# Kernel tuning notes

Hardware: AMD Instinct MI355X
Metric: run time of the kernel (lower is better)

Reference implementation:

```python
import jax, jax.numpy as jnp
import numpy as np

DIM = 768
NUM_HEADS = 12
HEAD_DIM = DIM // NUM_HEADS
SCALE = HEAD_DIM ** -0.5
NEG = -9e15


def setup_inputs() -> dict:
    key = jax.random.key(0)
    ks = jax.random.split(key, 8)
    B, N, M, C = 4, 1024, 2048, DIM
    q = jax.random.normal(ks[0], (B, N, C), dtype=jnp.float32)
    kv = jax.random.normal(ks[1], (B, M, C), dtype=jnp.float32)
    mask = jax.random.randint(ks[2], (B, 1, N, M), 0, 2, dtype=jnp.int32)
    s = 1.0 / np.sqrt(C)
    Wq = jax.random.normal(ks[3], (C, C), dtype=jnp.float32) * s      # nn.Linear(dim, dim), no bias
    Wkv = jax.random.normal(ks[4], (2 * C, C), dtype=jnp.float32) * s  # nn.Linear(dim, 2*dim), no bias
    Wproj = jax.random.normal(ks[5], (C, C), dtype=jnp.float32) * s
    bproj = jax.random.normal(ks[6], (C,), dtype=jnp.float32) * s
    return {"q": q, "kv": kv, "Wq": Wq, "Wkv": Wkv, "Wproj": Wproj, "bproj": bproj, "mask": mask}


def reference(q, kv, Wq, Wkv, Wproj, bproj, mask):
    B, M, C = kv.shape
    _, N, _ = q.shape
    H, d = NUM_HEADS, HEAD_DIM
    # kv projection -> [B, M, 2, H, d] -> k, v: [B, H, M, d]
    kvp = (kv @ Wkv.T).reshape(B, M, 2, H, d)
    k = kvp[:, :, 0].transpose(0, 2, 1, 3)
    v = kvp[:, :, 1].transpose(0, 2, 1, 3)
    # q projection -> [B, H, N, d], pre-scaled
    qp = (q @ Wq.T).reshape(B, N, H, d).transpose(0, 2, 1, 3) * SCALE
    attn = jnp.einsum('bhnd,bhmd->bhnm', qp, k)  # [B, H, N, M]
    attn = jnp.where(mask == 0, NEG, attn)
    attn = jax.nn.softmax(attn, axis=-1)
    # attn_drop / proj_drop have rate 0.0 (eval): identity
    x = jnp.einsum('bhnm,bhmd->bhnd', attn, v)
    x = x.transpose(0, 2, 1, 3).reshape(B, N, C)
    x = x @ Wproj.T + bproj
    return x
```

## Files before the change

kernel.cpp:

```cpp
#include <hip/hip_runtime.h>
#include <hip/hip_bf16.h>


typedef short    s16x8  __attribute__((ext_vector_type(8)));
typedef short    s16x4  __attribute__((ext_vector_type(4)));
typedef float    f32x4  __attribute__((ext_vector_type(4)));
typedef _Float16 f16x8  __attribute__((ext_vector_type(8)));
typedef _Float16 f16x4  __attribute__((ext_vector_type(4)));
typedef _Float16 f16x2  __attribute__((ext_vector_type(2)));

#define NUM_H 12
#define DIM   768
#define NQ    1024
#define MK    2048
#define QK_SCALE_LOG2E 0.18033688f

__device__ __forceinline__ short f2h(float v) {
    _Float16 h = (_Float16)v;
    return __builtin_bit_cast(short, h);
}
__device__ __forceinline__ f32x4 mfma16x32(f16x8 a, f16x8 b, f32x4 c) {
    return __builtin_amdgcn_mfma_f32_16x16x32_f16(a, b, c, 0, 0, 0);
}
__device__ __forceinline__ f32x4 mfma16x16(f16x4 a, f16x4 b, f32x4 c) {
    return __builtin_amdgcn_mfma_f32_16x16x16f16(a, b, c, 0, 0, 0);
}
__device__ __forceinline__ f16x2 pk2h(float a, float b) {
    return __builtin_bit_cast(f16x2, __builtin_amdgcn_cvt_pkrtz(a, b));
}

__global__ __launch_bounds__(256) void prep_kernel(
    const float* __restrict__ q, const float* __restrict__ kv,
    const float* __restrict__ Wq, const float* __restrict__ Wkv,
    const float* __restrict__ Wp, const int* __restrict__ mask,
    short* __restrict__ q_h, short* __restrict__ kv_h,
    short* __restrict__ Wq_h, short* __restrict__ Wkv_h,
    short* __restrict__ Wp_h, unsigned char* __restrict__ mbytes)
{
    int bid = blockIdx.x;
    if (bid < 5760) {
        const float* s; short* d; long base;
        if (bid < 1536)      { s = q;   d = q_h;   base = (long)bid * 2048; }
        else if (bid < 4608) { s = kv;  d = kv_h;  base = (long)(bid - 1536) * 2048; }
        else if (bid < 4896) { s = Wq;  d = Wq_h;  base = (long)(bid - 4608) * 2048; }
        else if (bid < 5472) { s = Wkv; d = Wkv_h; base = (long)(bid - 4896) * 2048; }
        else                 { s = Wp;  d = Wp_h;  base = (long)(bid - 5472) * 2048; }
        long i = base + threadIdx.x * 8;
        float4 a = *(const float4*)(s + i);
        float4 b = *(const float4*)(s + i + 4);
        s16x8 r;
        r[0] = f2h(a.x); r[1] = f2h(a.y); r[2] = f2h(a.z); r[3] = f2h(a.w);
        r[4] = f2h(b.x); r[5] = f2h(b.y); r[6] = f2h(b.z); r[7] = f2h(b.w);
        *(s16x8*)(d + i) = r;
    } else {
        long base = (long)(bid - 5760) * 2048 + threadIdx.x * 8;
        int4 m0 = *(const int4*)(mask + base);
        int4 m1 = *(const int4*)(mask + base + 4);
        unsigned v = (unsigned)(m0.x != 0)        | ((unsigned)(m0.y != 0) << 1)
                   | ((unsigned)(m0.z != 0) << 2) | ((unsigned)(m0.w != 0) << 3)
                   | ((unsigned)(m1.x != 0) << 4) | ((unsigned)(m1.y != 0) << 5)
                   | ((unsigned)(m1.z != 0) << 6) | ((unsigned)(m1.w != 0) << 7);
        mbytes[base >> 3] = (unsigned char)v;
    }
}

__device__ __forceinline__ void gemm_core(
    short* smem,
    const short* __restrict__ A, const short* __restrict__ Bt,
    int Ncols, int mode, const float* __restrict__ bias,
    short* __restrict__ outb, short* __restrict__ outb2,
    float* __restrict__ outf, int bid)
{
    short (*As)[72] = (short(*)[72])smem;
    short (*Bs)[72] = (short(*)[72])(smem + 9216);

    int ntiles = Ncols >> 7;
    int m0 = (bid / ntiles) << 7;
    int n0 = (bid % ntiles) << 7;
    int t = threadIdx.x;
    int w = t >> 6, lane = t & 63, quad = lane >> 4, l16 = lane & 15;
    int wm = (w & 1) << 6, wn = (w >> 1) << 6;

    f32x4 zero4 = {0.f, 0.f, 0.f, 0.f};
    f32x4 acc[4][4];
    for (int i = 0; i < 4; i++)
        for (int j = 0; j < 4; j++) acc[i][j] = zero4;

    int lr = t >> 1;
    int lc = (t & 1) << 5;
    const short* Ap = A + (long)(m0 + lr) * DIM + lc;
    const short* Bp = Bt + (long)(n0 + lr) * DIM + lc;

    s16x8 a8[4], b8[4];
    #pragma unroll
    for (int c = 0; c < 4; c++) {
        a8[c] = *(const s16x8*)(Ap + c * 8);
        b8[c] = *(const s16x8*)(Bp + c * 8);
    }

    for (int kt = 0; kt < DIM; kt += 64) {
        __syncthreads();
        #pragma unroll
        for (int c = 0; c < 4; c++) {
            *(s16x8*)&As[lr][lc + c * 8] = a8[c];
            *(s16x8*)&Bs[lr][lc + c * 8] = b8[c];
        }
        __syncthreads();
        if (kt + 64 < DIM) {
            #pragma unroll
            for (int c = 0; c < 4; c++) {
                a8[c] = *(const s16x8*)(Ap + kt + 64 + c * 8);
                b8[c] = *(const s16x8*)(Bp + kt + 64 + c * 8);
            }
        }
        #pragma unroll
        for (int kh = 0; kh < 2; kh++) {
            f16x8 af[4], bfr[4];
            #pragma unroll
            for (int i = 0; i < 4; i++) {
                s16x8 tmp = *(const s16x8*)&As[wm + i * 16 + l16][kh * 32 + quad * 8];
                af[i] = __builtin_bit_cast(f16x8, tmp);
            }
            #pragma unroll
            for (int j = 0; j < 4; j++) {
                s16x8 tmp = *(const s16x8*)&Bs[wn + j * 16 + l16][kh * 32 + quad * 8];
                bfr[j] = __builtin_bit_cast(f16x8, tmp);
            }
            #pragma unroll
            for (int i = 0; i < 4; i++)
                #pragma unroll
                for (int j = 0; j < 4; j++)
                    acc[i][j] = mfma16x32(af[i], bfr[j], acc[i][j]);
        }
    }

    __syncthreads();

    if (mode == 2) {
        #pragma unroll
        for (int i = 0; i < 4; i++)
            #pragma unroll
            for (int j = 0; j < 4; j++)
                #pragma unroll
                for (int r = 0; r < 4; r++) {
                    int row = m0 + wm + i * 16 + quad * 4 + r;
                    int col = n0 + wn + j * 16 + l16;
                    outf[(long)row * DIM + col] = acc[i][j][r] + bias[col];
                }
        return;
    }

    short (*Cs)[136] = (short(*)[136])smem;
    bool vreg = (mode == 1) && (n0 >= DIM);

    if (!vreg) {
        float sc = (mode == 0) ? QK_SCALE_LOG2E : 1.0f;
        #pragma unroll
        for (int i = 0; i < 4; i++)
            #pragma unroll
            for (int j = 0; j < 4; j++)
                #pragma unroll
                for (int r = 0; r < 4; r++)
                    Cs[wm + i * 16 + quad * 4 + r][wn + j * 16 + l16] =
                        f2h(acc[i][j][r] * sc);
    } else {
        #pragma unroll
        for (int i = 0; i < 4; i++)
            #pragma unroll
            for (int j = 0; j < 4; j++) {
                int c = wn + j * 16 + l16;
                int r0 = wm + i * 16 + quad * 4;
                s16x4 pk;
                pk[0] = f2h(acc[i][j][0]); pk[1] = f2h(acc[i][j][1]);
                pk[2] = f2h(acc[i][j][2]); pk[3] = f2h(acc[i][j][3]);
                *(s16x4*)&Cs[c][r0] = pk;
            }
    }
    __syncthreads();

    if (!vreg) {
        int hb2 = n0 >> 6;
        long rowsN = (mode == 0) ? NQ : MK;
        int b = (int)(m0 / rowsN);
        int rb = (int)(m0 % rowsN);
        short* ob0 = outb + ((long)(b * NUM_H + hb2) * rowsN + rb) * 64;
        short* ob1 = outb + ((long)(b * NUM_H + hb2 + 1) * rowsN + rb) * 64;
        #pragma unroll
        for (int k2 = 0; k2 < 8; k2++) {
            int ch = k2 * 256 + t;
            int half = ch >> 10, off = ch & 1023;
            s16x8 vd = *(const s16x8*)&Cs[off >> 3][(half << 6) + ((off & 7) << 3)];
            *(s16x8*)((half ? ob1 : ob0) + off * 8) = vd;
        }
    } else {
        int hb2 = (n0 - DIM) >> 6;
        int b = m0 >> 11, rb = m0 & 2047;
        #pragma unroll
        for (int k2 = 0; k2 < 8; k2++) {
            int ch = k2 * 256 + t;
            int c = ch >> 4, woff = (ch & 15) << 3;
            s16x8 vd = *(const s16x8*)&Cs[c][woff];
            int half = c >> 6, dd = c & 63;
            *(s16x8*)(outb2 + (((long)(b * NUM_H + hb2 + half) * 64 + dd) * MK + rb) + woff) = vd;
        }
    }
}

__global__ __launch_bounds__(256) void gemm12_kernel(
    const short* __restrict__ qh, const short* __restrict__ Wqh,
    const short* __restrict__ kvh, const short* __restrict__ Wkvh,
    short* __restrict__ qp, short* __restrict__ kk, short* __restrict__ vt)
{
    __shared__ short smem[18432];
    if (blockIdx.x < 192)
        gemm_core(smem, qh, Wqh, 768, 0, nullptr, qp, nullptr, nullptr, blockIdx.x);
    else
        gemm_core(smem, kvh, Wkvh, 1536, 1, nullptr, kk, vt, nullptr, blockIdx.x - 192);
}

__global__ __launch_bounds__(256) void gemm3_kernel(
    const short* __restrict__ xb, const short* __restrict__ Wph,
    const float* __restrict__ bias, float* __restrict__ out)
{
    __shared__ short smem[18432];
    gemm_core(smem, xb, Wph, 768, 2, bias, nullptr, nullptr, out, blockIdx.x);
}

__global__ __launch_bounds__(128) void attn_kernel(
    const short* __restrict__ qp, const short* __restrict__ kk,
    const short* __restrict__ vt, const unsigned* __restrict__ mb,
    short* __restrict__ xb)
{
    __shared__ short qs[64][72];
    __shared__ short ks[64][72];
    __shared__ short vs[64][72];

    int bid = blockIdx.x;
    int bh = bid % 48;
    int nt = bid / 48;
    int h = bh % NUM_H, b = bh / NUM_H;
    int n0 = nt << 6;
    int t = threadIdx.x, w = t >> 6, lane = t & 63, quad = lane >> 4, l16 = lane & 15;

    const short* qbase = qp + ((long)bh * NQ + n0) * 64;
    const short* kbase = kk + (long)bh * MK * 64;
    const short* vbase = vt + (long)bh * 64 * MK;
    const unsigned* mrow0 = mb + ((long)b * NQ + n0 + (w << 5) + l16) * 64;
    const unsigned* mrow1 = mrow0 + 16 * 64;

    int gr = t >> 3, gc = (t & 7) << 3;
    #pragma unroll
    for (int i = 0; i < 4; i++)
        *(s16x8*)&qs[gr + i * 16][gc] = *(const s16x8*)(qbase + (gr + i * 16) * 64 + gc);
    __syncthreads();

    f16x8 bq[2][2];
    #pragma unroll
    for (int s2 = 0; s2 < 2; s2++)
        #pragma unroll
        for (int kh = 0; kh < 2; kh++)
            bq[s2][kh] = __builtin_bit_cast(f16x8,
                *(const s16x8*)&qs[(w << 5) + (s2 << 4) + l16][kh * 32 + quad * 8]);

    s16x8 k8[4], v8[4];
    #pragma unroll
    for (int i = 0; i < 4; i++) {
        k8[i] = *(const s16x8*)(kbase + (long)(gr + i * 16) * 64 + gc);
        v8[i] = *(const s16x8*)(vbase + (long)(gr + i * 16) * MK + gc);
    }
    uint2 mw0 = *(const uint2*)(mrow0);
    uint2 mw1 = *(const uint2*)(mrow1);

    f32x4 zero4 = {0.f, 0.f, 0.f, 0.f};
    f32x4 o[2][4], ol[2];
    #pragma unroll
    for (int s2 = 0; s2 < 2; s2++) {
        ol[s2] = zero4;
        for (int j = 0; j < 4; j++) o[s2][j] = zero4;
    }
    const f16x4 ones = {(_Float16)1.f, (_Float16)1.f, (_Float16)1.f, (_Float16)1.f};

    for (int mt = 0; mt < MK; mt += 64) {
        __syncthreads();
        #pragma unroll
        for (int i = 0; i < 4; i++) {
            *(s16x8*)&ks[gr + i * 16][gc] = k8[i];
            *(s16x8*)&vs[gr + i * 16][gc] = v8[i];
        }
        unsigned cm[2][2] = {{mw0.x, mw0.y}, {mw1.x, mw1.y}};
        __syncthreads();
        if (mt + 64 < MK) {
            #pragma unroll
            for (int i = 0; i < 4; i++) {
                k8[i] = *(const s16x8*)(kbase + (long)(mt + 64 + gr + i * 16) * 64 + gc);
                v8[i] = *(const s16x8*)(vbase + (long)(gr + i * 16) * MK + mt + 64 + gc);
            }
            mw0 = *(const uint2*)(mrow0 + ((mt + 64) >> 5));
            mw1 = *(const uint2*)(mrow1 + ((mt + 64) >> 5));
        }

        f32x4 s[2][4];
        #pragma unroll
        for (int j = 0; j < 4; j++) { s[0][j] = zero4; s[1][j] = zero4; }
        #pragma unroll
        for (int kh = 0; kh < 2; kh++)
            #pragma unroll
            for (int j = 0; j < 4; j++) {
                f16x8 ak = __builtin_bit_cast(f16x8,
                    *(const s16x8*)&ks[j * 16 + l16][kh * 32 + quad * 8]);
                s[0][j] = mfma16x32(ak, bq[0][kh], s[0][j]);
                s[1][j] = mfma16x32(ak, bq[1][kh], s[1][j]);
            }

        f16x4 pa[2][4];
        #pragma unroll
        for (int s2 = 0; s2 < 2; s2++)
            #pragma unroll
            for (int j = 0; j < 4; j++) {
                unsigned wsel = (j < 2) ? cm[s2][0] : cm[s2][1];
                unsigned bits = wsel >> (((j & 1) << 4) + (quad << 2));
                float p0 = (bits & 1u)        ? __builtin_amdgcn_exp2f(s[s2][j][0]) : 0.f;
                float p1 = ((bits >> 1) & 1u) ? __builtin_amdgcn_exp2f(s[s2][j][1]) : 0.f;
                float p2 = ((bits >> 2) & 1u) ? __builtin_amdgcn_exp2f(s[s2][j][2]) : 0.f;
                float p3 = ((bits >> 3) & 1u) ? __builtin_amdgcn_exp2f(s[s2][j][3]) : 0.f;
                f16x2 lo = pk2h(p0, p1);
                f16x2 hi = pk2h(p2, p3);
                pa[s2][j] = __builtin_shufflevector(lo, hi, 0, 1, 2, 3);
            }

        #pragma unroll
        for (int j = 0; j < 4; j++) {
            ol[0] = mfma16x16(pa[0][j], ones, ol[0]);
            ol[1] = mfma16x16(pa[1][j], ones, ol[1]);
            #pragma unroll
            for (int jd = 0; jd < 4; jd++) {
                f16x4 bv = *(const f16x4*)&vs[jd * 16 + l16][j * 16 + quad * 4];
                o[0][jd] = mfma16x16(pa[0][j], bv, o[0][jd]);
                o[1][jd] = mfma16x16(pa[1][j], bv, o[1][jd]);
            }
        }
    }

    #pragma unroll
    for (int s2 = 0; s2 < 2; s2++) {
        float linv[4];
        #pragma unroll
        for (int rr = 0; rr < 4; rr++) linv[rr] = 1.0f / ol[s2][rr];
        #pragma unroll
        for (int jd = 0; jd < 4; jd++)
            #pragma unroll
            for (int rr = 0; rr < 4; rr++)
                qs[(w << 5) + (s2 << 4) + quad * 4 + rr][jd * 16 + l16] =
                    f2h(o[s2][jd][rr] * linv[rr]);
    }
    __syncthreads();
    #pragma unroll
    for (int k2 = 0; k2 < 4; k2++) {
        int row = (w << 5) + (lane >> 3) + k2 * 8;
        int cc = (lane & 7) << 3;
        s16x8 vd = *(const s16x8*)&qs[row][cc];
        *(s16x8*)(xb + ((long)b * NQ + n0 + row) * DIM + h * 64 + cc) = vd;
    }
}

extern "C" void kernel_launch(void* const* d_in, const int* in_sizes, int n_in,
                              void* d_out, int out_size, void* d_ws, size_t ws_size,
                              hipStream_t stream)
{
    const float* q     = (const float*)d_in[0];
    const float* kv    = (const float*)d_in[1];
    const float* Wq    = (const float*)d_in[2];
    const float* Wkv   = (const float*)d_in[3];
    const float* Wproj = (const float*)d_in[4];
    const float* bproj = (const float*)d_in[5];
    const int*   mask  = (const int*)d_in[6];
    float* out = (float*)d_out;

    char* ws = (char*)d_ws;
    short* q_h   = (short*)ws; ws += (size_t)4096 * 768 * 2;
    short* kv_h  = (short*)ws; ws += (size_t)8192 * 768 * 2;
    short* Wq_h  = (short*)ws; ws += (size_t)768 * 768 * 2;
    short* Wkv_h = (short*)ws; ws += (size_t)1536 * 768 * 2;
    short* Wp_h  = (short*)ws; ws += (size_t)768 * 768 * 2;
    short* qp    = (short*)ws; ws += (size_t)4096 * 768 * 2;
    short* kk    = (short*)ws; ws += (size_t)8192 * 768 * 2;
    short* vt    = (short*)ws; ws += (size_t)8192 * 768 * 2;
    short* xb    = (short*)ws; ws += (size_t)4096 * 768 * 2;
    unsigned char* mbytes = (unsigned char*)ws;

    prep_kernel<<<9856, 256, 0, stream>>>(q, kv, Wq, Wkv, Wproj, mask,
                                          q_h, kv_h, Wq_h, Wkv_h, Wp_h, mbytes);
    gemm12_kernel<<<960, 256, 0, stream>>>(q_h, Wq_h, kv_h, Wkv_h, qp, kk, vt);
    attn_kernel<<<768, 128, 0, stream>>>(qp, kk, vt, (const unsigned*)mbytes, xb);
    gemm3_kernel<<<192, 256, 0, stream>>>(xb, Wp_h, bproj, out);
}
```

Measured before the change: 226.5 us.

## Use 4 waves per attention block and 16x16x32 MFMA for PV

The attention kernel goes from 2 waves with 32 query rows each to 4 waves with 16 query rows each, doubling threads per block for the same 64-row tile. K rows are stored into shared memory with a permuted row order, so the score MFMA output lanes line up with the A-operand layout of a 16x16x32 MFMA. That lets the PV and row-sum products use the wider K=32 instruction instead of 16x16x16. The intent is more latency hiding and fewer MFMA issues. In exchange each wave reuses less of K/V from shared memory, and correctness depends on the permutation matching the mask bit layout.

New measurement: 216.4 us. 1.05x faster.

```diff
diff --git a/kernel.cpp b/kernel.cpp
--- a/kernel.cpp
+++ b/kernel.cpp
@@ -21,9 +21,6 @@
 }
 __device__ __forceinline__ f32x4 mfma16x32(f16x8 a, f16x8 b, f32x4 c) {
     return __builtin_amdgcn_mfma_f32_16x16x32_f16(a, b, c, 0, 0, 0);
-}
-__device__ __forceinline__ f32x4 mfma16x16(f16x4 a, f16x4 b, f32x4 c) {
-    return __builtin_amdgcn_mfma_f32_16x16x16f16(a, b, c, 0, 0, 0);
 }
 __device__ __forceinline__ f16x2 pk2h(float a, float b) {
     return __builtin_bit_cast(f16x2, __builtin_amdgcn_cvt_pkrtz(a, b));
@@ -226,7 +223,7 @@
     gemm_core(smem, xb, Wph, 768, 2, bias, nullptr, nullptr, out, blockIdx.x);
 }
 
-__global__ __launch_bounds__(128) void attn_kernel(
+__global__ __launch_bounds__(256) void attn_kernel(
     const short* __restrict__ qp, const short* __restrict__ kk,
     const short* __restrict__ vt, const unsigned* __restrict__ mb,
     short* __restrict__ xb)
@@ -245,121 +242,114 @@
     const short* qbase = qp + ((long)bh * NQ + n0) * 64;
     const short* kbase = kk + (long)bh * MK * 64;
     const short* vbase = vt + (long)bh * 64 * MK;
-    const unsigned* mrow0 = mb + ((long)b * NQ + n0 + (w << 5) + l16) * 64;
-    const unsigned* mrow1 = mrow0 + 16 * 64;
-
-    int gr = t >> 3, gc = (t & 7) << 3;
-    #pragma unroll
-    for (int i = 0; i < 4; i++)
-        *(s16x8*)&qs[gr + i * 16][gc] = *(const s16x8*)(qbase + (gr + i * 16) * 64 + gc);
+    const unsigned* mrow = mb + ((long)b * NQ + n0 + (w << 4) + l16) * 64;
+
+    {
+        int qr = t >> 2, c0 = (t & 3) << 4;
+        *(s16x8*)&qs[qr][c0]     = *(const s16x8*)(qbase + qr * 64 + c0);
+        *(s16x8*)&qs[qr][c0 + 8] = *(const s16x8*)(qbase + qr * 64 + c0 + 8);
+    }
     __syncthreads();
-
-    f16x8 bq[2][2];
-    #pragma unroll
-    for (int s2 = 0; s2 < 2; s2++)
-        #pragma unroll
-        for (int kh = 0; kh < 2; kh++)
-            bq[s2][kh] = __builtin_bit_cast(f16x8,
-                *(const s16x8*)&qs[(w << 5) + (s2 << 4) + l16][kh * 32 + quad * 8]);
-
-    s16x8 k8[4], v8[4];
-    #pragma unroll
-    for (int i = 0; i < 4; i++) {
-        k8[i] = *(const s16x8*)(kbase + (long)(gr + i * 16) * 64 + gc);
-        v8[i] = *(const s16x8*)(vbase + (long)(gr + i * 16) * MK + gc);
-    }
-    uint2 mw0 = *(const uint2*)(mrow0);
-    uint2 mw1 = *(const uint2*)(mrow1);
+    f16x8 bq[2];
+    #pragma unroll
+    for (int kh = 0; kh < 2; kh++)
+        bq[kh] = __builtin_bit_cast(f16x8,
+            *(const s16x8*)&qs[(w << 4) + l16][kh * 32 + quad * 8]);
+
+    int sr = t >> 2, c0 = (t & 3) << 4;
+    int pr = (sr & 32) + ((sr & 4) << 2) + ((sr & 24) >> 1) + (sr & 3);
+    const short* kp = kbase + (long)sr * 64 + c0;
+    const short* vp = vbase + (long)sr * MK + c0;
+
+    s16x8 k0 = *(const s16x8*)(kp);
+    s16x8 k1 = *(const s16x8*)(kp + 8);
+    s16x8 v0 = *(const s16x8*)(vp);
+    s16x8 v1 = *(const s16x8*)(vp + 8);
+    uint2 mwv = *(const uint2*)(mrow);
 
     f32x4 zero4 = {0.f, 0.f, 0.f, 0.f};
-    f32x4 o[2][4], ol[2];
-    #pragma unroll
-    for (int s2 = 0; s2 < 2; s2++) {
-        ol[s2] = zero4;
-        for (int j = 0; j < 4; j++) o[s2][j] = zero4;
-    }
-    const f16x4 ones = {(_Float16)1.f, (_Float16)1.f, (_Float16)1.f, (_Float16)1.f};
+    f32x4 o[4], ol = zero4;
+    for (int j = 0; j < 4; j++) o[j] = zero4;
+    const f16x8 ones = {(_Float16)1.f, (_Float16)1.f, (_Float16)1.f, (_Float16)1.f,
+                        (_Float16)1.f, (_Float16)1.f, (_Float16)1.f, (_Float16)1.f};
 
     for (int mt = 0; mt < MK; mt += 64) {
         __syncthreads();
-        #pragma unroll
-        for (int i = 0; i < 4; i++) {
-            *(s16x8*)&ks[gr + i * 16][gc] = k8[i];
-            *(s16x8*)&vs[gr + i * 16][gc] = v8[i];
-        }
-        unsigned cm[2][2] = {{mw0.x, mw0.y}, {mw1.x, mw1.y}};
+        *(s16x8*)&ks[pr][c0]     = k0;
+        *(s16x8*)&ks[pr][c0 + 8] = k1;
+        *(s16x8*)&vs[sr][c0]     = v0;
+        *(s16x8*)&vs[sr][c0 + 8] = v1;
+        unsigned cm0 = mwv.x, cm1 = mwv.y;
         __syncthreads();
         if (mt + 64 < MK) {
-            #pragma unroll
-            for (int i = 0; i < 4; i++) {
-                k8[i] = *(const s16x8*)(kbase + (long)(mt + 64 + gr + i * 16) * 64 + gc);
-                v8[i] = *(const s16x8*)(vbase + (long)(gr + i * 16) * MK + mt + 64 + gc);
-            }
-            mw0 = *(const uint2*)(mrow0 + ((mt + 64) >> 5));
-            mw1 = *(const uint2*)(mrow1 + ((mt + 64) >> 5));
-        }
-
-        f32x4 s[2][4];
-        #pragma unroll
-        for (int j = 0; j < 4; j++) { s[0][j] = zero4; s[1][j] = zero4; }
+            k0 = *(const s16x8*)(kp + (long)(mt + 64) * 64);
+            k1 = *(const s16x8*)(kp + (long)(mt + 64) * 64 + 8);
+            v0 = *(const s16x8*)(vp + mt + 64);
+            v1 = *(const s16x8*)(vp + mt + 64 + 8);
+            mwv = *(const uint2*)(mrow + ((mt + 64) >> 5));
+        }
+
+        f32x4 s[4];
+        #pragma unroll
+        for (int jj = 0; jj < 4; jj++) s[jj] = zero4;
         #pragma unroll
         for (int kh = 0; kh < 2; kh++)
             #pragma unroll
-            for (int j = 0; j < 4; j++) {
+            for (int jj = 0; jj < 4; jj++) {
                 f16x8 ak = __builtin_bit_cast(f16x8,
-                    *(const s16x8*)&ks[j * 16 + l16][kh * 32 + quad * 8]);
-                s[0][j] = mfma16x32(ak, bq[0][kh], s[0][j]);
-                s[1][j] = mfma16x32(ak, bq[1][kh], s[1][j]);
-            }
-
-        f16x4 pa[2][4];
-        #pragma unroll
-        for (int s2 = 0; s2 < 2; s2++)
-            #pragma unroll
-            for (int j = 0; j < 4; j++) {
-                unsigned wsel = (j < 2) ? cm[s2][0] : cm[s2][1];
-                unsigned bits = wsel >> (((j & 1) << 4) + (quad << 2));
-                float p0 = (bits & 1u)        ? __builtin_amdgcn_exp2f(s[s2][j][0]) : 0.f;
-                float p1 = ((bits >> 1) & 1u) ? __builtin_amdgcn_exp2f(s[s2][j][1]) : 0.f;
-                float p2 = ((bits >> 2) & 1u) ? __builtin_amdgcn_exp2f(s[s2][j][2]) : 0.f;
-                float p3 = ((bits >> 3) & 1u) ? __builtin_amdgcn_exp2f(s[s2][j][3]) : 0.f;
-                f16x2 lo = pk2h(p0, p1);
-                f16x2 hi = pk2h(p2, p3);
-                pa[s2][j] = __builtin_shufflevector(lo, hi, 0, 1, 2, 3);
-            }
-
-        #pragma unroll
-        for (int j = 0; j < 4; j++) {
-            ol[0] = mfma16x16(pa[0][j], ones, ol[0]);
-            ol[1] = mfma16x16(pa[1][j], ones, ol[1]);
+                    *(const s16x8*)&ks[jj * 16 + l16][kh * 32 + quad * 8]);
+                s[jj] = mfma16x32(ak, bq[kh], s[jj]);
+            }
+
+        f16x8 pa[2];
+        #pragma unroll
+        for (int j2 = 0; j2 < 2; j2++) {
+            unsigned wsel = j2 ? cm1 : cm0;
+            f16x2 pk[4];
+            #pragma unroll
+            for (int sub = 0; sub < 2; sub++) {
+                unsigned bits = wsel >> ((quad << 3) + (sub << 2));
+                const f32x4& sv = s[j2 * 2 + sub];
+                float p0 = (bits & 1u)        ? __builtin_amdgcn_exp2f(sv[0]) : 0.f;
+                float p1 = ((bits >> 1) & 1u) ? __builtin_amdgcn_exp2f(sv[1]) : 0.f;
+                float p2 = ((bits >> 2) & 1u) ? __builtin_amdgcn_exp2f(sv[2]) : 0.f;
+                float p3 = ((bits >> 3) & 1u) ? __builtin_amdgcn_exp2f(sv[3]) : 0.f;
+                pk[sub * 2]     = pk2h(p0, p1);
+                pk[sub * 2 + 1] = pk2h(p2, p3);
+            }
+            f16x4 lo = __builtin_shufflevector(pk[0], pk[1], 0, 1, 2, 3);
+            f16x4 hi = __builtin_shufflevector(pk[2], pk[3], 0, 1, 2, 3);
+            pa[j2] = __builtin_shufflevector(lo, hi, 0, 1, 2, 3, 4, 5, 6, 7);
+        }
+
+        #pragma unroll
+        for (int j2 = 0; j2 < 2; j2++) {
+            ol = mfma16x32(pa[j2], ones, ol);
             #pragma unroll
             for (int jd = 0; jd < 4; jd++) {
-                f16x4 bv = *(const f16x4*)&vs[jd * 16 + l16][j * 16 + quad * 4];
-                o[0][jd] = mfma16x16(pa[0][j], bv, o[0][jd]);
-                o[1][jd] = mfma16x16(pa[1][j], bv, o[1][jd]);
-            }
-        }
-    }
-
-    #pragma unroll
-    for (int s2 = 0; s2 < 2; s2++) {
-        float linv[4];
-        #pragma unroll
-        for (int rr = 0; rr < 4; rr++) linv[rr] = 1.0f / ol[s2][rr];
-        #pragma unroll
-        for (int jd = 0; jd < 4; jd++)
-            #pragma unroll
-            for (int rr = 0; rr < 4; rr++)
-                qs[(w << 5) + (s2 << 4) + quad * 4 + rr][jd * 16 + l16] =
-                    f2h(o[s2][jd][rr] * linv[rr]);
-    }
-    __syncthreads();
-    #pragma unroll
-    for (int k2 = 0; k2 < 4; k2++) {
-        int row = (w << 5) + (lane >> 3) + k2 * 8;
+                f16x8 bv = __builtin_bit_cast(f16x8,
+                    *(const s16x8*)&vs[jd * 16 + l16][j2 * 32 + quad * 8]);
+                o[jd] = mfma16x32(pa[j2], bv, o[jd]);
+            }
+        }
+    }
+
+    float linv[4];
+    #pragma unroll
+    for (int rr = 0; rr < 4; rr++) linv[rr] = 1.0f / ol[rr];
+    short (*ps)[72] = (short(*)[72])&qs[w << 4];
+    #pragma unroll
+    for (int jd = 0; jd < 4; jd++)
+        #pragma unroll
+        for (int rr = 0; rr < 4; rr++)
+            ps[quad * 4 + rr][jd * 16 + l16] = f2h(o[jd][rr] * linv[rr]);
+
+    #pragma unroll
+    for (int k2 = 0; k2 < 2; k2++) {
+        int row = (lane >> 3) + k2 * 8;
         int cc = (lane & 7) << 3;
-        s16x8 vd = *(const s16x8*)&qs[row][cc];
-        *(s16x8*)(xb + ((long)b * NQ + n0 + row) * DIM + h * 64 + cc) = vd;
+        s16x8 vd = *(const s16x8*)&ps[row][cc];
+        *(s16x8*)(xb + ((long)b * NQ + n0 + (w << 4) + row) * DIM + h * 64 + cc) = vd;
     }
 }
 
@@ -391,6 +381,6 @@
     prep_kernel<<<9856, 256, 0, stream>>>(q, kv, Wq, Wkv, Wproj, mask,
                                           q_h, kv_h, Wq_h, Wkv_h, Wp_h, mbytes);
     gemm12_kernel<<<960, 256, 0, stream>>>(q_h, Wq_h, kv_h, Wkv_h, qp, kk, vt);
-    attn_kernel<<<768, 128, 0, stream>>>(qp, kk, vt, (const unsigned*)mbytes, xb);
+    attn_kernel<<<768, 256, 0, stream>>>(qp, kk, vt, (const unsigned*)mbytes, xb);
     gemm3_kernel<<<192, 256, 0, stream>>>(xb, Wp_h, bproj, out);
 }
```
